# Kernel tuning notes

Measured on AMD Instinct MI355X. Metric: run time of the kernel, lower is better.

Reference implementation:

```python
import jax, jax.numpy as jnp
import numpy as np

B, L, D, H = 4, 1024, 1024, 16
DH = D // H  # 64
TOPK = 32


def setup_inputs() -> dict:
    key = jax.random.key(0)
    ks = jax.random.split(key, 9)
    s = 1.0 / np.sqrt(D)
    return {
        "x": jax.random.normal(ks[0], (B, L, D), jnp.float32),
        "Wq": jax.random.normal(ks[1], (D, D), jnp.float32) * s,
        "bq": jax.random.normal(ks[2], (D,), jnp.float32) * 0.01,
        "Wk": jax.random.normal(ks[3], (D, D), jnp.float32) * s,
        "bk": jax.random.normal(ks[4], (D,), jnp.float32) * 0.01,
        "Wv": jax.random.normal(ks[5], (D, D), jnp.float32) * s,
        "bv": jax.random.normal(ks[6], (D,), jnp.float32) * 0.01,
        "Wo": jax.random.normal(ks[7], (D, D), jnp.float32) * s,
        "bo": jax.random.normal(ks[8], (D,), jnp.float32) * 0.01,
        "top_k": TOPK,
    }


def reference(x, Wq, bq, Wk, bk, Wv, bv, Wo, bo, top_k):
    b, l, _ = x.shape
    q = (x @ Wq + bq).reshape(b, l, H, DH)
    k = (x @ Wk + bk).reshape(b, l, H, DH)
    v = (x @ Wv + bv).reshape(b, l, H, DH)
    # scores: [B, i, j, h]
    scores = jnp.einsum('bihd,bjhd->bijh', q, k) / np.sqrt(DH).astype(np.float32)
    # softmax over axis 2 (j), as in the original (dim=2 of bijh)
    weights = jax.nn.softmax(scores, axis=2)
    if top_k is not None:
        # top-k along j: move j to last axis -> [B, i, h, j]
        w_t = jnp.swapaxes(weights, 2, 3)
        _, idx = jax.lax.top_k(w_t, top_k)
        mask = jnp.put_along_axis(jnp.zeros_like(w_t), idx, 1.0, axis=-1, inplace=False)
        w_t = w_t * mask
        w_t = w_t / (jnp.sum(w_t, axis=-1, keepdims=True) + 1e-8)
        weights = jnp.swapaxes(w_t, 2, 3)
    attn = jnp.einsum('bijh,bjhd->bihd', weights, v).reshape(b, l, D)
    return attn @ Wo + bo
```

## Files before the change

kernel.cpp:

```cpp
#include <hip/hip_runtime.h>
#include <math.h>

#define B_ 4
#define L_ 1024
#define D_ 1024
#define H_ 16
#define DH_ 64
#define M_ (B_*L_)

typedef _Float16 half8 __attribute__((ext_vector_type(8)));
typedef _Float16 half4 __attribute__((ext_vector_type(4)));
typedef float f32x4 __attribute__((ext_vector_type(4)));

#define MFMA16(a,b,c) __builtin_amdgcn_mfma_f32_16x16x32_f16(a, b, c, 0, 0, 0)

__global__ __launch_bounds__(256) void split_x(const float* __restrict__ x,
                                               _Float16* __restrict__ xh,
                                               _Float16* __restrict__ xl) {
  const int i = blockIdx.x * 256 + threadIdx.x;
  float4 v = ((const float4*)x)[i];
  const float a0 = v.x * 16.f, a1 = v.y * 16.f, a2 = v.z * 16.f, a3 = v.w * 16.f;
  const _Float16 h0 = (_Float16)a0, h1 = (_Float16)a1, h2 = (_Float16)a2, h3 = (_Float16)a3;
  half4 hv, lv;
  hv[0] = h0; hv[1] = h1; hv[2] = h2; hv[3] = h3;
  lv[0] = (_Float16)(a0 - (float)h0);
  lv[1] = (_Float16)(a1 - (float)h1);
  lv[2] = (_Float16)(a2 - (float)h2);
  lv[3] = (_Float16)(a3 - (float)h3);
  ((half4*)xh)[i] = hv;
  ((half4*)xl)[i] = lv;
}

__global__ __launch_bounds__(256) void split_wt(const float* __restrict__ W,
                                                _Float16* __restrict__ Wh,
                                                _Float16* __restrict__ Wl) {
  __shared__ float tile[64][65];
  const int t = threadIdx.x;
  const int tk = blockIdx.x & 15;
  const int tn = blockIdx.x >> 4;
  const int kr = t >> 2, ns = (t & 3) * 16;
  const float* src = W + (size_t)(tk * 64 + kr) * D_ + tn * 64 + ns;
  float4 v0 = ((const float4*)src)[0];
  float4 v1 = ((const float4*)src)[1];
  float4 v2 = ((const float4*)src)[2];
  float4 v3 = ((const float4*)src)[3];
  tile[ns + 0][kr] = v0.x;  tile[ns + 1][kr] = v0.y;  tile[ns + 2][kr] = v0.z;  tile[ns + 3][kr] = v0.w;
  tile[ns + 4][kr] = v1.x;  tile[ns + 5][kr] = v1.y;  tile[ns + 6][kr] = v1.z;  tile[ns + 7][kr] = v1.w;
  tile[ns + 8][kr] = v2.x;  tile[ns + 9][kr] = v2.y;  tile[ns + 10][kr] = v2.z; tile[ns + 11][kr] = v2.w;
  tile[ns + 12][kr] = v3.x; tile[ns + 13][kr] = v3.y; tile[ns + 14][kr] = v3.z; tile[ns + 15][kr] = v3.w;
  __syncthreads();
  const int nr = t >> 2, ks = (t & 3) * 16;
  const float* tr = &tile[nr][ks];
  half8 hv0, hv1, lv0, lv1;
#pragma unroll
  for (int i = 0; i < 8; i++) {
    const float s0 = tr[i] * 512.f;
    const float s1 = tr[i + 8] * 512.f;
    const _Float16 h0 = (_Float16)s0, h1 = (_Float16)s1;
    hv0[i] = h0; hv1[i] = h1;
    lv0[i] = (_Float16)(s0 - (float)h0);
    lv1[i] = (_Float16)(s1 - (float)h1);
  }
  _Float16* dh = Wh + (size_t)(tn * 64 + nr) * D_ + tk * 64 + ks;
  _Float16* dl = Wl + (size_t)(tn * 64 + nr) * D_ + tk * 64 + ks;
  *(half8*)dh = hv0; *(half8*)(dh + 8) = hv1;
  *(half8*)dl = lv0; *(half8*)(dl + 8) = lv1;
}

__device__ __forceinline__ void gemm_f16x3_body(
    const _Float16* __restrict__ Ah, const _Float16* __restrict__ Al,
    const _Float16* __restrict__ Bh, const _Float16* __restrict__ Bl,
    const float* __restrict__ bias, float* __restrict__ Cf,
    _Float16* __restrict__ Ch, _Float16* __restrict__ Cl, const bool f16out) {
  __shared__ __align__(16) _Float16 sA[2][2][128][32];
  __shared__ __align__(16) _Float16 sB[2][2][128][32];
  const int t = threadIdx.x;
  const int lane = t & 63;
  const int wid = t >> 6;
  const int bm = blockIdx.y * 128;
  const int bn = blockIdx.x * 128;

  const int m0 = t >> 2, sp0 = t & 3;
  const int sl0 = sp0 ^ ((m0 >> 1) & 3);
  const int m1 = m0 + 64;
  const _Float16* gA0h = Ah + (size_t)(bm + m0) * D_ + sl0 * 8;
  const _Float16* gA1h = Ah + (size_t)(bm + m1) * D_ + sl0 * 8;
  const _Float16* gA0l = Al + (size_t)(bm + m0) * D_ + sl0 * 8;
  const _Float16* gA1l = Al + (size_t)(bm + m1) * D_ + sl0 * 8;
  const _Float16* gB0h = Bh + (size_t)(bn + m0) * D_ + sl0 * 8;
  const _Float16* gB1h = Bh + (size_t)(bn + m1) * D_ + sl0 * 8;
  const _Float16* gB0l = Bl + (size_t)(bn + m0) * D_ + sl0 * 8;
  const _Float16* gB1l = Bl + (size_t)(bn + m1) * D_ + sl0 * 8;

  half8 rA0h = *(const half8*)(gA0h);
  half8 rA1h = *(const half8*)(gA1h);
  half8 rA0l = *(const half8*)(gA0l);
  half8 rA1l = *(const half8*)(gA1l);
  half8 rB0h = *(const half8*)(gB0h);
  half8 rB1h = *(const half8*)(gB1h);
  half8 rB0l = *(const half8*)(gB0l);
  half8 rB1l = *(const half8*)(gB1l);
  *(half8*)&sA[0][0][m0][sp0 * 8] = rA0h;
  *(half8*)&sA[0][0][m1][sp0 * 8] = rA1h;
  *(half8*)&sA[0][1][m0][sp0 * 8] = rA0l;
  *(half8*)&sA[0][1][m1][sp0 * 8] = rA1l;
  *(half8*)&sB[0][0][m0][sp0 * 8] = rB0h;
  *(half8*)&sB[0][0][m1][sp0 * 8] = rB1h;
  *(half8*)&sB[0][1][m0][sp0 * 8] = rB0l;
  *(half8*)&sB[0][1][m1][sp0 * 8] = rB1l;
  __syncthreads();

  f32x4 acc[4][4];
#pragma unroll
  for (int i = 0; i < 4; i++)
#pragma unroll
    for (int j = 0; j < 4; j++) acc[i][j] = {0.f, 0.f, 0.f, 0.f};

  const int wr = wid >> 1, wc = wid & 1;
  const int l15 = lane & 15;
  const int soff = ((lane >> 4) ^ ((l15 >> 1) & 3)) * 8;

  int p = 0;
  for (int k0 = 0; k0 < 1024; k0 += 32) {
    const bool more = (k0 + 32) < 1024;
    if (more) {
      const int kk = k0 + 32;
      rA0h = *(const half8*)(gA0h + kk);
      rA1h = *(const half8*)(gA1h + kk);
      rA0l = *(const half8*)(gA0l + kk);
      rA1l = *(const half8*)(gA1l + kk);
      rB0h = *(const half8*)(gB0h + kk);
      rB1h = *(const half8*)(gB1h + kk);
      rB0l = *(const half8*)(gB0l + kk);
      rB1l = *(const half8*)(gB1l + kk);
    }
    half8 bh[4], bl[4];
#pragma unroll
    for (int ni = 0; ni < 4; ni++) {
      const int rb = wc * 64 + ni * 16 + l15;
      bh[ni] = *(const half8*)&sB[p][0][rb][soff];
      bl[ni] = *(const half8*)&sB[p][1][rb][soff];
    }
#pragma unroll
    for (int mi = 0; mi < 4; mi++) {
      const int ra = wr * 64 + mi * 16 + l15;
      const half8 ah = *(const half8*)&sA[p][0][ra][soff];
      const half8 al = *(const half8*)&sA[p][1][ra][soff];
#pragma unroll
      for (int ni = 0; ni < 4; ni++) {
        acc[mi][ni] = MFMA16(ah, bh[ni], acc[mi][ni]);
        acc[mi][ni] = MFMA16(ah, bl[ni], acc[mi][ni]);
        acc[mi][ni] = MFMA16(al, bh[ni], acc[mi][ni]);
      }
    }
    if (more) {
      const int q = p ^ 1;
      *(half8*)&sA[q][0][m0][sp0 * 8] = rA0h;
      *(half8*)&sA[q][0][m1][sp0 * 8] = rA1h;
      *(half8*)&sA[q][1][m0][sp0 * 8] = rA0l;
      *(half8*)&sA[q][1][m1][sp0 * 8] = rA1l;
      *(half8*)&sB[q][0][m0][sp0 * 8] = rB0h;
      *(half8*)&sB[q][0][m1][sp0 * 8] = rB1h;
      *(half8*)&sB[q][1][m0][sp0 * 8] = rB0l;
      *(half8*)&sB[q][1][m1][sp0 * 8] = rB1l;
      __syncthreads();
      p = q;
    }
  }

  const float inv = 1.0f / 8192.0f;
  const int orow = bm + wr * 64 + (lane >> 4) * 4;
  const int ocol = bn + wc * 64 + l15;
#pragma unroll
  for (int ni = 0; ni < 4; ni++) {
    const int col = ocol + ni * 16;
    const float bv = bias[col];
#pragma unroll
    for (int mi = 0; mi < 4; mi++) {
      const f32x4 a = acc[mi][ni];
#pragma unroll
      for (int r = 0; r < 4; r++) {
        const size_t idx = (size_t)(orow + mi * 16 + r) * D_ + col;
        const float val = a[r] * inv + bv;
        if (f16out) {
          const float vs = val * 16.0f;
          const _Float16 hh = (_Float16)vs;
          Ch[idx] = hh;
          Cl[idx] = (_Float16)(vs - (float)hh);
        } else {
          Cf[idx] = val;
        }
      }
    }
  }
}

__global__ __launch_bounds__(256, 2) void gemm_qkv_f16(
    const _Float16* __restrict__ xh, const _Float16* __restrict__ xl,
    const _Float16* __restrict__ Whq, const _Float16* __restrict__ Wlq,
    const _Float16* __restrict__ Whk, const _Float16* __restrict__ Wlk,
    const _Float16* __restrict__ Whv, const _Float16* __restrict__ Wlv,
    const float* __restrict__ bq, const float* __restrict__ bk, const float* __restrict__ bv,
    _Float16* __restrict__ qh, _Float16* __restrict__ ql,
    _Float16* __restrict__ kh, _Float16* __restrict__ kl,
    float* __restrict__ vf) {
  const int z = blockIdx.z;
  const _Float16* Bh = (z == 0) ? Whq : (z == 1) ? Whk : Whv;
  const _Float16* Bl = (z == 0) ? Wlq : (z == 1) ? Wlk : Wlv;
  const float* bias = (z == 0) ? bq : (z == 1) ? bk : bv;
  if (z == 2) {
    gemm_f16x3_body(xh, xl, Bh, Bl, bias, vf, nullptr, nullptr, false);
  } else {
    _Float16* Ch = (z == 0) ? qh : kh;
    _Float16* Cl = (z == 0) ? ql : kl;
    gemm_f16x3_body(xh, xl, Bh, Bl, bias, nullptr, Ch, Cl, true);
  }
}

__global__ __launch_bounds__(256, 2) void gemm_out_f16(
    const _Float16* __restrict__ ah, const _Float16* __restrict__ al,
    const _Float16* __restrict__ bh, const _Float16* __restrict__ bl,
    const float* __restrict__ bias, float* __restrict__ C) {
  gemm_f16x3_body(ah, al, bh, bl, bias, C, nullptr, nullptr, false);
}

#define SSWZ(row) (((row) & 7) << 2)

__global__ __launch_bounds__(512, 4) void attn_topk_mfma(
    const _Float16* __restrict__ qh, const _Float16* __restrict__ ql,
    const _Float16* __restrict__ kh, const _Float16* __restrict__ kl,
    const float* __restrict__ vf,
    _Float16* __restrict__ awh, _Float16* __restrict__ awl) {
  __shared__ float S[8][1024];
  __shared__ int   cidx[8][64];
  __shared__ float cfe[8][64];
  const int t = threadIdx.x;
  const int lane = t & 63;
  const int w = t >> 6;
  const int i0 = blockIdx.x * 8;
  const int h = blockIdx.y;
  const int b = blockIdx.z;
  const size_t rowbase = (size_t)b * L_;
  const int l15 = lane & 15;
  const int kgrp = lane >> 4;

  half8 Ahf[2], Alf[2];
#pragma unroll
  for (int ks = 0; ks < 2; ks++) {
    const size_t off = (rowbase + i0 + (l15 & 7)) * D_ + h * DH_ + ks * 32 + kgrp * 8;
    Ahf[ks] = *(const half8*)(qh + off);
    Alf[ks] = *(const half8*)(ql + off);
  }

  const float sscale = 1.0f / 2048.0f;
  for (int jt = 0; jt < 8; jt++) {
    const int j0 = w * 128 + jt * 16;
    const size_t koff = (rowbase + j0 + l15) * D_ + h * DH_ + kgrp * 8;
    const half8 Bh0 = *(const half8*)(kh + koff);
    const half8 Bh1 = *(const half8*)(kh + koff + 32);
    const half8 Bl0 = *(const half8*)(kl + koff);
    const half8 Bl1 = *(const half8*)(kl + koff + 32);
    f32x4 acc = {0.f, 0.f, 0.f, 0.f};
    acc = MFMA16(Ahf[0], Bh0, acc);
    acc = MFMA16(Ahf[1], Bh1, acc);
    acc = MFMA16(Ahf[0], Bl0, acc);
    acc = MFMA16(Ahf[1], Bl1, acc);
    acc = MFMA16(Alf[0], Bh0, acc);
    acc = MFMA16(Alf[1], Bh1, acc);
    if (kgrp < 2) {
      const int srow = kgrp * 4;
#pragma unroll
      for (int r = 0; r < 4; r++)
        S[srow + r][(j0 + l15) ^ SSWZ(srow + r)] = acc[r] * sscale;
    }
  }
  __syncthreads();

  const int row = w;
  const int swz = SSWZ(row);
  float sc[16];
#pragma unroll
  for (int u = 0; u < 16; u++) sc[u] = S[row][(u * 64 + lane) ^ swz];

  float mx = sc[0];
#pragma unroll
  for (int u = 1; u < 16; u++) mx = fmaxf(mx, sc[u]);
#pragma unroll
  for (int off = 32; off >= 1; off >>= 1) mx = fmaxf(mx, __shfl_xor(mx, off, 64));

  float lo = mx - 16.f, hi = mx;
  for (int it = 0; it < 14; ++it) {
    float mid = 0.5f * (lo + hi);
    int cnt = 0;
#pragma unroll
    for (int u = 0; u < 16; u++) cnt += __popcll(__ballot(sc[u] >= mid));
    if (cnt >= 32) lo = mid; else hi = mid;
  }
  int cabove = 0;
#pragma unroll
  for (int u = 0; u < 16; u++) cabove += __popcll(__ballot(sc[u] >= hi));
  float v31 = hi;
  while (cabove < 32) {
    float nx = -INFINITY;
#pragma unroll
    for (int u = 0; u < 16; u++) nx = fmaxf(nx, (sc[u] < v31) ? sc[u] : -INFINITY);
#pragma unroll
    for (int off = 32; off >= 1; off >>= 1) nx = fmaxf(nx, __shfl_xor(nx, off, 64));
    int ceq = 0;
#pragma unroll
    for (int u = 0; u < 16; u++) ceq += __popcll(__ballot(sc[u] == nx));
    cabove += ceq;
    v31 = nx;
  }
  int c_eq = 0;
#pragma unroll
  for (int u = 0; u < 16; u++) c_eq += __popcll(__ballot(sc[u] == v31));
  const int c_gt = cabove - c_eq;
  const bool span = (cabove > 32);
  const int keep_eq = 32 - c_gt;
  float v32;
  if (span) {
    v32 = v31;
  } else {
    float nx = -INFINITY;
#pragma unroll
    for (int u = 0; u < 16; u++) nx = fmaxf(nx, (sc[u] < v31) ? sc[u] : -INFINITY);
#pragma unroll
    for (int off = 32; off >= 1; off >>= 1) nx = fmaxf(nx, __shfl_xor(nx, off, 64));
    v32 = nx;
  }
  const float tau = 0.5f * (v31 + v32);
  const float invbeta = 166666.67f;

  float z = 0.f;
#pragma unroll
  for (int u = 0; u < 16; u++) z += __expf(sc[u] - mx);
#pragma unroll
  for (int off = 32; off >= 1; off >>= 1) z += __shfl_xor(z, off, 64);

  bool band = false;
  if (!span) {
    int inband = 0;
#pragma unroll
    for (int u = 0; u < 16; u++)
      inband |= (fabsf(sc[u] - tau) <= 1.81e-4f) ? 1 : 0;
    band = (__ballot(inband) != 0ull);
  }

  const float cutoff = fminf(tau - 1.8e-4f, v31);
  const float* vcol = vf + rowbase * D_ + h * DH_ + lane;
  float o;
  bool fast = false;
  if (!span) {
    int run = 0;
    float psum = 0.f;
#pragma unroll
    for (int u = 0; u < 16; u++) {
      unsigned long long m = __ballot(sc[u] >= cutoff);
      if (sc[u] >= cutoff) {
        const float eu = __expf(sc[u] - mx);
        float feu;
        if (band) {
          float arg = (sc[u] - tau) * invbeta;
          float fwv = (arg > 30.f) ? 1.f : ((arg < -30.f) ? 0.f : 1.f / (1.f + __expf(-arg)));
          feu = fwv * eu;
        } else {
          feu = (sc[u] > tau) ? eu : 0.f;
        }
        int pos = run + (int)__popcll(m & ((1ull << lane) - 1ull));
        if (pos < 64) { cidx[w][pos] = u * 64 + lane; cfe[w][pos] = feu; }
        psum += feu;
      }
      run += (int)__popcll(m);
    }
    if (run <= 64) {
      fast = true;
      float Ssum = psum;
#pragma unroll
      for (int off = 32; off >= 1; off >>= 1) Ssum += __shfl_xor(Ssum, off, 64);
      const int npad = (run + 7) & ~7;
      if (lane < npad - run) { cidx[w][run + lane] = 0; cfe[w][run + lane] = 0.f; }
      float acc = 0.f;
      for (int c = 0; c < npad; c += 8) {
        int jx[8]; float fx[8]; float vv[8];
#pragma unroll
        for (int i = 0; i < 8; i++) { jx[i] = cidx[w][c + i]; fx[i] = cfe[w][c + i]; }
#pragma unroll
        for (int i = 0; i < 8; i++) vv[i] = vcol[(size_t)jx[i] * D_];
#pragma unroll
        for (int i = 0; i < 8; i++) acc = fmaf(fx[i], vv[i], acc);
      }
      o = acc / (Ssum + 1e-8f * z);
    }
  }
  if (!fast) {
    float Ssum = 0.f, acc = 0.f;
    int eq_seen = 0;
    for (int u = 0; u < 16; ++u) {
      unsigned long long mask = __ballot(sc[u] >= cutoff);
      while (mask) {
        int l2 = (int)__builtin_ctzll(mask);
        mask &= mask - 1;
        float s_ = __shfl(sc[u], l2, 64);
        float e_ = __expf(s_ - mx);
        float f_;
        if (span) {
          if (s_ > v31) f_ = 1.f;
          else if (s_ == v31) { f_ = (eq_seen < keep_eq) ? 1.f : 0.f; ++eq_seen; }
          else f_ = 0.f;
        } else {
          float arg = (s_ - tau) * invbeta;
          f_ = (arg > 30.f) ? 1.f : ((arg < -30.f) ? 0.f : 1.f / (1.f + __expf(-arg)));
        }
        float fe_ = f_ * e_;
        Ssum += fe_;
        acc = fmaf(fe_, vcol[(size_t)(u * 64 + l2) * D_], acc);
      }
    }
    o = acc / (Ssum + 1e-8f * z);
  }

  const float os = o * 16.0f;
  const _Float16 oh = (_Float16)os;
  const size_t oidx = (rowbase + i0 + row) * D_ + h * DH_ + lane;
  awh[oidx] = oh;
  awl[oidx] = (_Float16)(os - (float)oh);
}

extern "C" void kernel_launch(void* const* d_in, const int* in_sizes, int n_in,
                              void* d_out, int out_size, void* d_ws, size_t ws_size,
                              hipStream_t stream) {
  const float* x  = (const float*)d_in[0];
  const float* Wq = (const float*)d_in[1];
  const float* bq = (const float*)d_in[2];
  const float* Wk = (const float*)d_in[3];
  const float* bk = (const float*)d_in[4];
  const float* Wv = (const float*)d_in[5];
  const float* bv = (const float*)d_in[6];
  const float* Wo = (const float*)d_in[7];
  const float* bo = (const float*)d_in[8];
  float* out = (float*)d_out;

  const size_t MD = (size_t)M_ * D_;
  const size_t WD = (size_t)D_ * D_;
  float* slot0 = (float*)d_ws;
  float* slot1 = slot0 + MD;
  float* vf    = slot1 + MD;
  float* slot3 = vf + MD;
  float* slot4 = slot3 + MD;

  _Float16* qh = (_Float16*)slot0;  _Float16* ql = qh + MD;
  _Float16* kh = (_Float16*)slot1;  _Float16* kl = kh + MD;
  _Float16* xh = (_Float16*)slot3;  _Float16* xl = xh + MD;
  _Float16* awh = xh;
  _Float16* awl = xl;
  _Float16* Whq = (_Float16*)slot4;
  _Float16* Wlq = Whq + WD;
  _Float16* Whk = Wlq + WD;
  _Float16* Wlk = Whk + WD;
  _Float16* Whv = Wlk + WD;
  _Float16* Wlv = Whv + WD;
  _Float16* Who = Wlv + WD;
  _Float16* Wlo = Who + WD;

  dim3 b256(256);
  hipLaunchKernelGGL(split_x, dim3(4096), b256, 0, stream, x, xh, xl);
  hipLaunchKernelGGL(split_wt, dim3(256), b256, 0, stream, Wq, Whq, Wlq);
  hipLaunchKernelGGL(split_wt, dim3(256), b256, 0, stream, Wk, Whk, Wlk);
  hipLaunchKernelGGL(split_wt, dim3(256), b256, 0, stream, Wv, Whv, Wlv);
  hipLaunchKernelGGL(split_wt, dim3(256), b256, 0, stream, Wo, Who, Wlo);
  hipLaunchKernelGGL(gemm_qkv_f16, dim3(8, 32, 3), b256, 0, stream,
                     xh, xl, Whq, Wlq, Whk, Wlk, Whv, Wlv, bq, bk, bv,
                     qh, ql, kh, kl, vf);
  hipLaunchKernelGGL(attn_topk_mfma, dim3(128, 16, 4), dim3(512), 0, stream,
                     qh, ql, kh, kl, vf, awh, awl);
  hipLaunchKernelGGL(gemm_out_f16, dim3(8, 32), b256, 0, stream,
                     awh, awl, Who, Wlo, bo, out);
}
```

Before: 500.6 us.

## Shrink attention blocks to 4 query rows, DPP reductions, XCD-aware block mapping, merged weight splits

The attention kernel now processes 4 query rows per 256-thread block instead of 8 rows per 512-thread block. It uses a flat grid with a remap that interleaves work across the 8 XCDs, and it drops the shared-memory swizzle. Wavefront max/sum reductions switch from shuffle-xor loops to DPP row operations plus a readlane. The four weight-split launches are merged into one launch over a z-dimension. The cost is that each block recomputes QK MFMAs over twice as many key tiles per query row, and only a quarter of the MFMA output rows are used.

```diff
diff --git a/kernel.cpp b/kernel.cpp
--- a/kernel.cpp
+++ b/kernel.cpp
@@ -13,6 +13,28 @@
 typedef float f32x4 __attribute__((ext_vector_type(4)));
 
 #define MFMA16(a,b,c) __builtin_amdgcn_mfma_f32_16x16x32_f16(a, b, c, 0, 0, 0)
+
+#define DPPF(oldv, x, ctrl, rmask) \
+  __int_as_float(__builtin_amdgcn_update_dpp(__float_as_int(oldv), __float_as_int(x), ctrl, rmask, 0xf, false))
+
+__device__ __forceinline__ float wfred_max(float x) {
+  x = fmaxf(x, DPPF(-INFINITY, x, 0x111, 0xf));
+  x = fmaxf(x, DPPF(-INFINITY, x, 0x112, 0xf));
+  x = fmaxf(x, DPPF(-INFINITY, x, 0x114, 0xf));
+  x = fmaxf(x, DPPF(-INFINITY, x, 0x118, 0xf));
+  x = fmaxf(x, DPPF(-INFINITY, x, 0x142, 0xa));
+  x = fmaxf(x, DPPF(-INFINITY, x, 0x143, 0xc));
+  return __int_as_float(__builtin_amdgcn_readlane(__float_as_int(x), 63));
+}
+__device__ __forceinline__ float wfred_sum(float x) {
+  x = x + DPPF(0.f, x, 0x111, 0xf);
+  x = x + DPPF(0.f, x, 0x112, 0xf);
+  x = x + DPPF(0.f, x, 0x114, 0xf);
+  x = x + DPPF(0.f, x, 0x118, 0xf);
+  x = x + DPPF(0.f, x, 0x142, 0xa);
+  x = x + DPPF(0.f, x, 0x143, 0xc);
+  return __int_as_float(__builtin_amdgcn_readlane(__float_as_int(x), 63));
+}
 
 __global__ __launch_bounds__(256) void split_x(const float* __restrict__ x,
                                                _Float16* __restrict__ xh,
@@ -31,9 +53,15 @@
   ((half4*)xl)[i] = lv;
 }
 
-__global__ __launch_bounds__(256) void split_wt(const float* __restrict__ W,
-                                                _Float16* __restrict__ Wh,
-                                                _Float16* __restrict__ Wl) {
+__global__ __launch_bounds__(256) void split_w4(const float* __restrict__ W0,
+                                                const float* __restrict__ W1,
+                                                const float* __restrict__ W2,
+                                                const float* __restrict__ W3,
+                                                _Float16* __restrict__ Whl_base) {
+  const int z = blockIdx.z;
+  const float* W = (z == 0) ? W0 : (z == 1) ? W1 : (z == 2) ? W2 : W3;
+  _Float16* Wh = Whl_base + (size_t)z * 2 * (size_t)(D_ * D_);
+  _Float16* Wl = Wh + (size_t)(D_ * D_);
   __shared__ float tile[64][65];
   const int t = threadIdx.x;
   const int tk = blockIdx.x & 15;
@@ -224,22 +252,24 @@
   gemm_f16x3_body(ah, al, bh, bl, bias, C, nullptr, nullptr, false);
 }
 
-#define SSWZ(row) (((row) & 7) << 2)
-
-__global__ __launch_bounds__(512, 4) void attn_topk_mfma(
+__global__ __launch_bounds__(256, 8) void attn_topk_mfma(
     const _Float16* __restrict__ qh, const _Float16* __restrict__ ql,
     const _Float16* __restrict__ kh, const _Float16* __restrict__ kl,
     const float* __restrict__ vf,
     _Float16* __restrict__ awh, _Float16* __restrict__ awl) {
-  __shared__ float S[8][1024];
-  __shared__ int   cidx[8][64];
-  __shared__ float cfe[8][64];
+  __shared__ float S[4][1024];
+  __shared__ int   cidx[4][64];
+  __shared__ float cfe[4][64];
   const int t = threadIdx.x;
   const int lane = t & 63;
   const int w = t >> 6;
-  const int i0 = blockIdx.x * 8;
-  const int h = blockIdx.y;
-  const int b = blockIdx.z;
+  const int id = blockIdx.x;
+  const int wk = (id & 7) * 2048 + (id >> 3);
+  const int it = wk & 255;
+  const int bh = wk >> 8;
+  const int h = bh & 15;
+  const int b = bh >> 4;
+  const int i0 = it * 4;
   const size_t rowbase = (size_t)b * L_;
   const int l15 = lane & 15;
   const int kgrp = lane >> 4;
@@ -247,14 +277,14 @@
   half8 Ahf[2], Alf[2];
 #pragma unroll
   for (int ks = 0; ks < 2; ks++) {
-    const size_t off = (rowbase + i0 + (l15 & 7)) * D_ + h * DH_ + ks * 32 + kgrp * 8;
+    const size_t off = (rowbase + i0 + (l15 & 3)) * D_ + h * DH_ + ks * 32 + kgrp * 8;
     Ahf[ks] = *(const half8*)(qh + off);
     Alf[ks] = *(const half8*)(ql + off);
   }
 
   const float sscale = 1.0f / 2048.0f;
-  for (int jt = 0; jt < 8; jt++) {
-    const int j0 = w * 128 + jt * 16;
+  for (int jt = 0; jt < 16; jt++) {
+    const int j0 = w * 256 + jt * 16;
     const size_t koff = (rowbase + j0 + l15) * D_ + h * DH_ + kgrp * 8;
     const half8 Bh0 = *(const half8*)(kh + koff);
     const half8 Bh1 = *(const half8*)(kh + koff + 32);
@@ -267,29 +297,29 @@
     acc = MFMA16(Ahf[1], Bl1, acc);
     acc = MFMA16(Alf[0], Bh0, acc);
     acc = MFMA16(Alf[1], Bh1, acc);
-    if (kgrp < 2) {
-      const int srow = kgrp * 4;
+    if (kgrp == 0) {
 #pragma unroll
       for (int r = 0; r < 4; r++)
-        S[srow + r][(j0 + l15) ^ SSWZ(srow + r)] = acc[r] * sscale;
+        S[r][j0 + l15] = acc[r] * sscale;
     }
   }
   __syncthreads();
 
   const int row = w;
-  const int swz = SSWZ(row);
   float sc[16];
 #pragma unroll
-  for (int u = 0; u < 16; u++) sc[u] = S[row][(u * 64 + lane) ^ swz];
-
-  float mx = sc[0];
-#pragma unroll
-  for (int u = 1; u < 16; u++) mx = fmaxf(mx, sc[u]);
-#pragma unroll
-  for (int off = 32; off >= 1; off >>= 1) mx = fmaxf(mx, __shfl_xor(mx, off, 64));
+  for (int u = 0; u < 16; u++) sc[u] = S[row][u * 64 + lane];
+
+  float mx;
+  {
+    float m = sc[0];
+#pragma unroll
+    for (int u = 1; u < 16; u++) m = fmaxf(m, sc[u]);
+    mx = wfred_max(m);
+  }
 
   float lo = mx - 16.f, hi = mx;
-  for (int it = 0; it < 14; ++it) {
+  for (int it2 = 0; it2 < 14; ++it2) {
     float mid = 0.5f * (lo + hi);
     int cnt = 0;
 #pragma unroll
@@ -304,8 +334,7 @@
     float nx = -INFINITY;
 #pragma unroll
     for (int u = 0; u < 16; u++) nx = fmaxf(nx, (sc[u] < v31) ? sc[u] : -INFINITY);
-#pragma unroll
-    for (int off = 32; off >= 1; off >>= 1) nx = fmaxf(nx, __shfl_xor(nx, off, 64));
+    nx = wfred_max(nx);
     int ceq = 0;
 #pragma unroll
     for (int u = 0; u < 16; u++) ceq += __popcll(__ballot(sc[u] == nx));
@@ -325,8 +354,7 @@
     float nx = -INFINITY;
 #pragma unroll
     for (int u = 0; u < 16; u++) nx = fmaxf(nx, (sc[u] < v31) ? sc[u] : -INFINITY);
-#pragma unroll
-    for (int off = 32; off >= 1; off >>= 1) nx = fmaxf(nx, __shfl_xor(nx, off, 64));
+    nx = wfred_max(nx);
     v32 = nx;
   }
   const float tau = 0.5f * (v31 + v32);
@@ -335,8 +363,7 @@
   float z = 0.f;
 #pragma unroll
   for (int u = 0; u < 16; u++) z += __expf(sc[u] - mx);
-#pragma unroll
-  for (int off = 32; off >= 1; off >>= 1) z += __shfl_xor(z, off, 64);
+  z = wfred_sum(z);
 
   bool band = false;
   if (!span) {
@@ -368,23 +395,21 @@
           feu = (sc[u] > tau) ? eu : 0.f;
         }
         int pos = run + (int)__popcll(m & ((1ull << lane) - 1ull));
-        if (pos < 64) { cidx[w][pos] = u * 64 + lane; cfe[w][pos] = feu; }
+        if (pos < 64) { cidx[row][pos] = u * 64 + lane; cfe[row][pos] = feu; }
         psum += feu;
       }
       run += (int)__popcll(m);
     }
     if (run <= 64) {
       fast = true;
-      float Ssum = psum;
-#pragma unroll
-      for (int off = 32; off >= 1; off >>= 1) Ssum += __shfl_xor(Ssum, off, 64);
+      const float Ssum = wfred_sum(psum);
       const int npad = (run + 7) & ~7;
-      if (lane < npad - run) { cidx[w][run + lane] = 0; cfe[w][run + lane] = 0.f; }
+      if (lane < npad - run) { cidx[row][run + lane] = 0; cfe[row][run + lane] = 0.f; }
       float acc = 0.f;
       for (int c = 0; c < npad; c += 8) {
         int jx[8]; float fx[8]; float vv[8];
 #pragma unroll
-        for (int i = 0; i < 8; i++) { jx[i] = cidx[w][c + i]; fx[i] = cfe[w][c + i]; }
+        for (int i = 0; i < 8; i++) { jx[i] = cidx[row][c + i]; fx[i] = cfe[row][c + i]; }
 #pragma unroll
         for (int i = 0; i < 8; i++) vv[i] = vcol[(size_t)jx[i] * D_];
 #pragma unroll
@@ -454,7 +479,8 @@
   _Float16* xh = (_Float16*)slot3;  _Float16* xl = xh + MD;
   _Float16* awh = xh;
   _Float16* awl = xl;
-  _Float16* Whq = (_Float16*)slot4;
+  _Float16* Wsplit = (_Float16*)slot4;
+  _Float16* Whq = Wsplit;
   _Float16* Wlq = Whq + WD;
   _Float16* Whk = Wlq + WD;
   _Float16* Wlk = Whk + WD;
@@ -465,14 +491,11 @@
 
   dim3 b256(256);
   hipLaunchKernelGGL(split_x, dim3(4096), b256, 0, stream, x, xh, xl);
-  hipLaunchKernelGGL(split_wt, dim3(256), b256, 0, stream, Wq, Whq, Wlq);
-  hipLaunchKernelGGL(split_wt, dim3(256), b256, 0, stream, Wk, Whk, Wlk);
-  hipLaunchKernelGGL(split_wt, dim3(256), b256, 0, stream, Wv, Whv, Wlv);
-  hipLaunchKernelGGL(split_wt, dim3(256), b256, 0, stream, Wo, Who, Wlo);
+  hipLaunchKernelGGL(split_w4, dim3(256, 1, 4), b256, 0, stream, Wq, Wk, Wv, Wo, Wsplit);
   hipLaunchKernelGGL(gemm_qkv_f16, dim3(8, 32, 3), b256, 0, stream,
                      xh, xl, Whq, Wlq, Whk, Wlk, Whv, Wlv, bq, bk, bv,
                      qh, ql, kh, kl, vf);
-  hipLaunchKernelGGL(attn_topk_mfma, dim3(128, 16, 4), dim3(512), 0, stream,
+  hipLaunchKernelGGL(attn_topk_mfma, dim3(16384), b256, 0, stream,
                      qh, ql, kh, kl, vf, awh, awl);
   hipLaunchKernelGGL(gemm_out_f16, dim3(8, 32), b256, 0, stream,
                      awh, awl, Who, Wlo, bo, out);
```

Result: slower. 722.4 us (+44.3%).
